# Optimization experiments

Measured on AMD Instinct MI355X. Metric: run time of the kernel, lower is better.

## Reference

```python
import jax, jax.numpy as jnp
import numpy as np

D_MODEL = 1024
HIDDEN = 512
NUM_EXPERTS = 16
TOP_K = 2
CAP_FACTOR = 1.25
ALPHA = 0.01


def setup_inputs() -> dict:
    key = jax.random.key(0)
    ks = jax.random.split(key, 10)
    s_in = 1.0 / np.sqrt(D_MODEL)
    s_h = 1.0 / np.sqrt(HIDDEN)
    return {
        "x": jax.random.normal(ks[0], (4, 4096, D_MODEL), dtype=jnp.float32),
        "gate_w": jax.random.normal(ks[1], (D_MODEL, NUM_EXPERTS), dtype=jnp.float32) * s_in,
        "gate_b": jnp.zeros((NUM_EXPERTS,), dtype=jnp.float32),
        "gp_w": jax.random.normal(ks[2], (NUM_EXPERTS, D_MODEL, HIDDEN), dtype=jnp.float32) * s_in,
        "gp_b": jnp.zeros((NUM_EXPERTS, HIDDEN), dtype=jnp.float32),
        "up_w": jax.random.normal(ks[3], (NUM_EXPERTS, D_MODEL, HIDDEN), dtype=jnp.float32) * s_in,
        "up_b": jnp.zeros((NUM_EXPERTS, HIDDEN), dtype=jnp.float32),
        "dp_w": jax.random.normal(ks[4], (NUM_EXPERTS, HIDDEN, D_MODEL), dtype=jnp.float32) * s_h,
        "dp_b": jnp.zeros((NUM_EXPERTS, D_MODEL), dtype=jnp.float32),
    }


def reference(x, gate_w, gate_b, gp_w, gp_b, up_w, up_b, dp_w, dp_b):
    B, S, D = x.shape
    T = B * S
    xf = x.reshape(T, D)

    # --- MoEGate ---
    logits = xf @ gate_w + gate_b                      # [T, E]
    scores = jax.nn.softmax(logits, axis=-1)
    topk_w, topk_i = jax.lax.top_k(scores, TOP_K)      # [T, K]
    # norm_topk_prob=True in DeepSeekMoE
    topk_w = topk_w / (jnp.sum(topk_w, axis=-1, keepdims=True) + 1e-9)

    one_hot = jax.nn.one_hot(topk_i, NUM_EXPERTS, dtype=jnp.float32)  # [T, K, E]
    load = jnp.sum(one_hot, axis=(0, 1))               # [E]
    capacity = CAP_FACTOR * (T * TOP_K) / NUM_EXPERTS
    capacity_penalty = jnp.sum(jax.nn.relu(load - capacity)) / NUM_EXPERTS / T
    aux_loss = ALPHA * capacity_penalty

    # combine weight of expert e for each token: [T, E]
    comb = jnp.einsum("tke,tk->te", one_hot, topk_w)

    # --- dispatch/combine (dense per-expert, weighted by comb) ---
    out = jnp.zeros_like(xf)
    for e in range(NUM_EXPERTS):
        # Expert: down_proj(gate_proj(x) * silu(up_proj(x)))
        h = (xf @ gp_w[e] + gp_b[e]) * jax.nn.silu(xf @ up_w[e] + up_b[e])
        y = h @ dp_w[e] + dp_b[e]
        out = out + comb[:, e:e + 1] * y

    return out.reshape(B, S, D), aux_loss
```

## Files before the change

kernel.cpp:

```cpp
#include <hip/hip_runtime.h>
#include <hip/hip_bf16.h>
#include <math.h>

#define T_TOK 16384
#define DMODEL 1024
#define HID 512
#define NEXP 16
#define NASSIGN (T_TOK * 2)
#define HIST_BLK 64
#define TOK_PER_BLK (T_TOK / HIST_BLK)
#define NMB_MAX 143

typedef __bf16 bf16_8 __attribute__((ext_vector_type(8)));
typedef __bf16 bf16_4 __attribute__((ext_vector_type(4)));
typedef float f32_4 __attribute__((ext_vector_type(4)));

__device__ __forceinline__ void gload16(const __bf16* g, __bf16* l) {
  __builtin_amdgcn_global_load_lds(
      (const __attribute__((address_space(1))) void*)g,
      (__attribute__((address_space(3))) void*)l, 16, 0, 0);
}

__global__ __launch_bounds__(256) void gate_compute_kernel(
    const float* __restrict__ x, const float* __restrict__ gw, const float* __restrict__ gb,
    __bf16* __restrict__ xb, int* __restrict__ topk_idx, float2* __restrict__ topk_w)
{
  __shared__ __align__(16) float gws[4 * 1024 * 4];

  int tid = threadIdx.x;
#pragma unroll
  for (int i = 0; i < 16; ++i) {
    int c = i * 256 + tid;
    f32_4 v = ((const f32_4*)gw)[c];
    ((f32_4*)gws)[((c & 3) << 10) | (c >> 2)] = v;
  }
  __syncthreads();

  int wave = tid >> 6, lane = tid & 63;
  int tbase = blockIdx.x * 32 + wave * 8;

#pragma unroll 1
  for (int pass = 0; pass < 2; ++pass) {
    int t0 = tbase + pass * 4;
    const float* xr0 = x + (size_t)t0 * DMODEL;
    const float* xr1 = xr0 + DMODEL;
    const float* xr2 = xr1 + DMODEL;
    const float* xr3 = xr2 + DMODEL;
    __bf16* xw0 = xb + (size_t)t0 * DMODEL;
    __bf16* xw1 = xw0 + DMODEL;
    __bf16* xw2 = xw1 + DMODEL;
    __bf16* xw3 = xw2 + DMODEL;

    f32_4 acc0[4], acc1[4], acc2[4], acc3[4];
    {
      f32_4 z = {0.f, 0.f, 0.f, 0.f};
#pragma unroll
      for (int g = 0; g < 4; ++g) { acc0[g] = z; acc1[g] = z; acc2[g] = z; acc3[g] = z; }
    }

#pragma unroll
    for (int j = 0; j < 16; ++j) {
      int k = j * 64 + lane;
      float xv0 = xr0[k], xv1 = xr1[k], xv2 = xr2[k], xv3 = xr3[k];
      xw0[k] = (__bf16)xv0;
      xw1[k] = (__bf16)xv1;
      xw2[k] = (__bf16)xv2;
      xw3[k] = (__bf16)xv3;
      f32_4 w0 = ((const f32_4*)gws)[k];
      f32_4 w1 = ((const f32_4*)gws)[1024 + k];
      f32_4 w2 = ((const f32_4*)gws)[2048 + k];
      f32_4 w3 = ((const f32_4*)gws)[3072 + k];
      acc0[0] += xv0 * w0; acc0[1] += xv0 * w1; acc0[2] += xv0 * w2; acc0[3] += xv0 * w3;
      acc1[0] += xv1 * w0; acc1[1] += xv1 * w1; acc1[2] += xv1 * w2; acc1[3] += xv1 * w3;
      acc2[0] += xv2 * w0; acc2[1] += xv2 * w1; acc2[2] += xv2 * w2; acc2[3] += xv2 * w3;
      acc3[0] += xv3 * w0; acc3[1] += xv3 * w1; acc3[2] += xv3 * w2; acc3[3] += xv3 * w3;
    }

#pragma unroll
    for (int g = 0; g < 4; ++g)
#pragma unroll
      for (int w = 0; w < 4; ++w) {
        float v0 = acc0[g][w], v1 = acc1[g][w], v2 = acc2[g][w], v3 = acc3[g][w];
#pragma unroll
        for (int s = 32; s; s >>= 1) {
          v0 += __shfl_xor(v0, s, 64);
          v1 += __shfl_xor(v1, s, 64);
          v2 += __shfl_xor(v2, s, 64);
          v3 += __shfl_xor(v3, s, 64);
        }
        acc0[g][w] = v0; acc1[g][w] = v1; acc2[g][w] = v2; acc3[g][w] = v3;
      }

    int ti = lane & 3;
    float sc[16];
#pragma unroll
    for (int e = 0; e < 16; ++e) {
      int g = e >> 2, w = e & 3;
      float v = ti == 0 ? acc0[g][w] : ti == 1 ? acc1[g][w] : ti == 2 ? acc2[g][w] : acc3[g][w];
      sc[e] = v + gb[e];
    }
    float mx = -1e30f;
#pragma unroll
    for (int e = 0; e < 16; ++e) mx = fmaxf(mx, sc[e]);
    float Z = 0.f;
#pragma unroll
    for (int e = 0; e < 16; ++e) { sc[e] = expf(sc[e] - mx); Z += sc[e]; }
    int i0 = 0; float s0 = sc[0];
#pragma unroll
    for (int e = 1; e < 16; ++e) if (sc[e] > s0) { s0 = sc[e]; i0 = e; }
    int i1 = -1; float s1 = -1e30f;
#pragma unroll
    for (int e = 0; e < 16; ++e) if (e != i0 && sc[e] > s1) { s1 = sc[e]; i1 = e; }
    s0 /= Z; s1 /= Z;
    float dn = s0 + s1 + 1e-9f;
    if (lane < 4) {
      int t = t0 + ti;
      topk_idx[t] = i0 | (i1 << 8);
      topk_w[t] = make_float2(s0 / dn, s1 / dn);
    }
  }
}

__global__ __launch_bounds__(256) void hist_kernel(
    const int* __restrict__ topk_idx, int* __restrict__ block_hist)
{
  __shared__ int cnt[NEXP];
  int tid = threadIdx.x;
  if (tid < NEXP) cnt[tid] = 0;
  __syncthreads();
  int t = blockIdx.x * TOK_PER_BLK + tid;
  int p = topk_idx[t];
  atomicAdd(&cnt[p & 0xff], 1);
  atomicAdd(&cnt[p >> 8], 1);
  __syncthreads();
  if (tid < NEXP) block_hist[blockIdx.x * NEXP + tid] = cnt[tid];
}

__global__ void scan2_kernel(const int* __restrict__ block_hist,
                             int* __restrict__ counts, int* __restrict__ offsets,
                             int* __restrict__ block_base, int* __restrict__ mb_tab,
                             int* __restrict__ nmb, float* __restrict__ aux_out)
{
  __shared__ int cl[NEXP];
  int lane = threadIdx.x;
  if (lane < NEXP) {
    int s = 0;
    for (int b = 0; b < HIST_BLK; ++b) s += block_hist[b * NEXP + lane];
    cl[lane] = s;
    counts[lane] = s;
  }
  __syncthreads();
  if (lane < NEXP) {
    int off = 0;
    for (int e = 0; e < lane; ++e) off += cl[e];
    offsets[lane] = off;
    int base = off;
    for (int b = 0; b < HIST_BLK; ++b) {
      block_base[b * NEXP + lane] = base;
      base += block_hist[b * NEXP + lane];
    }
  }
  if (lane == 0) {
    int tot = 0; float pen = 0.f;
    const float cap = 1.25f * (float)(T_TOK * 2) / (float)NEXP;
    for (int e = 0; e < NEXP; ++e) {
      tot += cl[e];
      float ld = (float)cl[e] - cap;
      pen += ld > 0.f ? ld : 0.f;
    }
    offsets[NEXP] = tot;
    aux_out[0] = 0.01f * pen / (float)NEXP / (float)T_TOK;
    int idx = 0;
    for (int e = 0; e < NEXP; ++e) {
      int nb = (cl[e] + 255) >> 8;
      for (int b = 0; b < nb; ++b) mb_tab[idx++] = (e << 8) | b;
    }
    nmb[0] = idx;
  }
}

__global__ __launch_bounds__(256) void scatter_kernel(
    const int* __restrict__ topk_idx, const int* __restrict__ block_base,
    int* __restrict__ tok_list, int2* __restrict__ tok_slots)
{
  __shared__ int base[NEXP];
  int tid = threadIdx.x;
  if (tid < NEXP) base[tid] = block_base[blockIdx.x * NEXP + tid];
  __syncthreads();
  int t = blockIdx.x * TOK_PER_BLK + tid;
  int p = topk_idx[t];
  int i0 = p & 0xff, i1 = p >> 8;
  int p0 = atomicAdd(&base[i0], 1);
  tok_list[p0] = t;
  int p1 = atomicAdd(&base[i1], 1);
  tok_list[p1] = t;
  tok_slots[t] = make_int2(p0, p1);
}

__global__ __launch_bounds__(256) void transpose_w1_kernel(const float* __restrict__ gp,
                                                           const float* __restrict__ up,
                                                           __bf16* __restrict__ wb1)
{
  __shared__ float tile[32][33];
  int ez = blockIdx.z;
  int e = ez >> 1, isup = ez & 1;
  const float* in = isup ? up : gp;
  int c0 = blockIdx.x * 32, r0 = blockIdx.y * 32;
  const float* src = in + ((size_t)e * 1024 + r0) * 512 + c0;
#pragma unroll
  for (int i = 0; i < 4; ++i) {
    int r = threadIdx.y + i * 8;
    tile[r][threadIdx.x] = src[(size_t)r * 512 + threadIdx.x];
  }
  __syncthreads();
#pragma unroll
  for (int i = 0; i < 4; ++i) {
    int cc = threadIdx.y + i * 8;
    int np = 2 * c0 + 2 * (cc & ~15) + (cc & 15) + 16 * isup;
    wb1[((size_t)e * 1024 + np) * 1024 + r0 + threadIdx.x] = (__bf16)tile[threadIdx.x][cc];
  }
}

__global__ __launch_bounds__(256) void transpose_dp_kernel(const float* __restrict__ in,
                                                           __bf16* __restrict__ out)
{
  __shared__ float tile[32][33];
  int e = blockIdx.z;
  int c0 = blockIdx.x * 32, r0 = blockIdx.y * 32;
  const float* src = in + ((size_t)e * 512 + r0) * 1024 + c0;
#pragma unroll
  for (int i = 0; i < 4; ++i) {
    int r = threadIdx.y + i * 8;
    tile[r][threadIdx.x] = src[(size_t)r * 1024 + threadIdx.x];
  }
  __syncthreads();
  __bf16* dst = out + ((size_t)e * 1024 + c0) * 512 + r0;
#pragma unroll
  for (int i = 0; i < 4; ++i) {
    int c = threadIdx.y + i * 8;
    dst[(size_t)c * 512 + threadIdx.x] = (__bf16)tile[threadIdx.x][c];
  }
}


#define PHASE_MID()                                          \
  __builtin_amdgcn_sched_barrier(0);                         \
  __builtin_amdgcn_s_barrier();                              \
  asm volatile("s_waitcnt lgkmcnt(0)" ::: "memory");         \
  __builtin_amdgcn_sched_barrier(0);                         \
  __builtin_amdgcn_s_setprio(1);

#define PHASE_END()                                          \
  __builtin_amdgcn_s_setprio(0);                             \
  __builtin_amdgcn_sched_barrier(0);                         \
  __builtin_amdgcn_s_barrier();

#define MF(mi, ni, a, b) acc[mi][ni] = __builtin_amdgcn_mfma_f32_16x16x32_bf16(a, b, acc[mi][ni], 0, 0, 0)

#define STAGE_A(b, kt) {                                          \
    gload16(ga0 + (kt) * 32, lds + (b) * 16384 + tid * 8);        \
    gload16(ga1 + (kt) * 32, lds + (b) * 16384 + 4096 + tid * 8); }
#define STAGE_B(b, kt) {                                          \
    gload16(gb0 + (kt) * 32, lds + (b) * 16384 + 8192 + tid * 8); \
    gload16(gb1 + (kt) * 32, lds + (b) * 16384 + 12288 + tid * 8); }

#define GTILE(ktv, STG)                                                           \
  {                                                                               \
    const __bf16* A_ = lds + ((ktv) & 1) * 16384;                                 \
    const __bf16* B_ = A_ + 8192;                                                 \
    bf16_8 af0, af1, af2, af3, bf0, bf1, bf2, bf3;                                \
    af0 = *(const bf16_8*)(A_ + abase + 0 * 512 + sq);                            \
    af1 = *(const bf16_8*)(A_ + abase + 1 * 512 + sq);                            \
    af2 = *(const bf16_8*)(A_ + abase + 2 * 512 + sq);                            \
    af3 = *(const bf16_8*)(A_ + abase + 3 * 512 + sq);                            \
    bf0 = *(const bf16_8*)(B_ + bbase + 0 * 512 + sq);                            \
    bf1 = *(const bf16_8*)(B_ + bbase + 1 * 512 + sq);                            \
    bf2 = *(const bf16_8*)(B_ + bbase + 2 * 512 + sq);                            \
    bf3 = *(const bf16_8*)(B_ + bbase + 3 * 512 + sq);                            \
    if (STG) STAGE_A(((ktv) + 1) & 1, (ktv) + 1);                                 \
    PHASE_MID();                                                                  \
    MF(0, 0, af0, bf0); MF(0, 1, af0, bf1); MF(0, 2, af0, bf2); MF(0, 3, af0, bf3); \
    MF(1, 0, af1, bf0); MF(1, 1, af1, bf1); MF(1, 2, af1, bf2); MF(1, 3, af1, bf3); \
    MF(2, 0, af2, bf0); MF(2, 1, af2, bf1); MF(2, 2, af2, bf2); MF(2, 3, af2, bf3); \
    MF(3, 0, af3, bf0); MF(3, 1, af3, bf1); MF(3, 2, af3, bf2); MF(3, 3, af3, bf3); \
    PHASE_END();                                                                  \
    af0 = *(const bf16_8*)(A_ + abase + 4 * 512 + sq);                            \
    af1 = *(const bf16_8*)(A_ + abase + 5 * 512 + sq);                            \
    af2 = *(const bf16_8*)(A_ + abase + 6 * 512 + sq);                            \
    af3 = *(const bf16_8*)(A_ + abase + 7 * 512 + sq);                            \
    if (STG) STAGE_B(((ktv) + 1) & 1, (ktv) + 1);                                 \
    PHASE_MID();                                                                  \
    MF(4, 0, af0, bf0); MF(4, 1, af0, bf1); MF(4, 2, af0, bf2); MF(4, 3, af0, bf3); \
    MF(5, 0, af1, bf0); MF(5, 1, af1, bf1); MF(5, 2, af1, bf2); MF(5, 3, af1, bf3); \
    MF(6, 0, af2, bf0); MF(6, 1, af2, bf1); MF(6, 2, af2, bf2); MF(6, 3, af2, bf3); \
    MF(7, 0, af3, bf0); MF(7, 1, af3, bf1); MF(7, 2, af3, bf2); MF(7, 3, af3, bf3); \
    __builtin_amdgcn_s_setprio(0);                                                \
    __builtin_amdgcn_sched_barrier(0);                                            \
    if (STG) { asm volatile("s_waitcnt vmcnt(0)" ::: "memory"); }                 \
    __builtin_amdgcn_sched_barrier(0);                                            \
    __builtin_amdgcn_s_barrier();                                                 \
  }

template<int KTILES>
__device__ __forceinline__ void gemm8w(
    const __bf16* ga0, const __bf16* ga1,
    const __bf16* gb0, const __bf16* gb1,
    __bf16* lds, f32_4 (&acc)[8][4])
{
  const int tid = threadIdx.x;
  const int wid = tid >> 6, wr = wid >> 2, wc = wid & 3;
  const int lane = tid & 63, quad = lane >> 4, l16 = lane & 15;
  const int sq = (quad ^ ((l16 >> 1) & 3)) * 8;
  const int abase = (wr * 128 + l16) * 32;
  const int bbase = (wc * 64 + l16) * 32;

  STAGE_A(0, 0); STAGE_B(0, 0);
  asm volatile("s_waitcnt vmcnt(0)" ::: "memory");
  __builtin_amdgcn_sched_barrier(0);
  __builtin_amdgcn_s_barrier();

#pragma unroll 1
  for (int kt = 0; kt < KTILES - 1; ++kt) {
    GTILE(kt, 1);
  }
  GTILE(KTILES - 1, 0);
}

__global__ __launch_bounds__(512, 2) void ffn1_kernel(
    const __bf16* __restrict__ xb, const __bf16* __restrict__ wb1,
    const float* __restrict__ gp_b, const float* __restrict__ up_b,
    const int* __restrict__ counts, const int* __restrict__ offsets,
    const int* __restrict__ tok_list, const int* __restrict__ mb_tab,
    const int* __restrict__ nmb, __bf16* __restrict__ h)
{
  __shared__ __align__(16) __bf16 lds[2 * 16384];
  __shared__ int toks[256];

  int lin = blockIdx.y * 4 + blockIdx.x;
  int xcd = lin & 7, sub = lin >> 3;
  int wg = (xcd < 4 ? xcd * 72 : 288 + (xcd - 4) * 71) + sub;
  int y = wg >> 2, xn = wg & 3;
  if (y >= nmb[0]) return;
  int me = mb_tab[y];
  int e = me >> 8;
  int m0 = (me & 255) << 8;
  int cnt = counts[e], offe = offsets[e];
  int n0 = xn * 256;

  int tid = threadIdx.x;
  if (tid < 256) {
    int r = m0 + tid;
    toks[tid] = tok_list[offe + (r < cnt ? r : cnt - 1)];
  }
  __syncthreads();

  int rr = tid >> 2;
  int ko = ((tid & 3) ^ ((rr >> 1) & 3)) * 8;

  const __bf16* ga0 = xb + (size_t)toks[rr] * DMODEL + ko;
  const __bf16* ga1 = xb + (size_t)toks[128 + rr] * DMODEL + ko;
  const __bf16* gb0 = wb1 + ((size_t)e * 1024 + n0 + rr) * DMODEL + ko;
  const __bf16* gb1 = wb1 + ((size_t)e * 1024 + n0 + 128 + rr) * DMODEL + ko;

  f32_4 acc[8][4];
  {
    f32_4 z = {0.f, 0.f, 0.f, 0.f};
#pragma unroll
    for (int a = 0; a < 8; ++a)
#pragma unroll
      for (int b = 0; b < 4; ++b) acc[a][b] = z;
  }

  gemm8w<DMODEL / 32>(ga0, ga1, gb0, gb1, lds, acc);

  int wid = tid >> 6, wr = wid >> 2, wc = wid & 3;
  int lane = tid & 63, quad = lane >> 4, l16 = lane & 15;

#pragma unroll
  for (int mi = 0; mi < 8; ++mi)
#pragma unroll
    for (int j = 0; j < 2; ++j) {
      int c = (n0 >> 1) + wc * 32 + j * 16 + l16;
      float gbias = gp_b[e * HID + c];
      float ubias = up_b[e * HID + c];
#pragma unroll
      for (int rg = 0; rg < 4; ++rg) {
        int r = m0 + wr * 128 + mi * 16 + quad * 4 + rg;
        if (r < cnt) {
          float g = acc[mi][2 * j][rg] + gbias;
          float u = acc[mi][2 * j + 1][rg] + ubias;
          float sw = u / (1.f + expf(-u));
          h[(size_t)(offe + r) * HID + c] = (__bf16)(g * sw);
        }
      }
    }
}

__global__ __launch_bounds__(512, 2) void ffn2_kernel(
    const __bf16* __restrict__ h, const __bf16* __restrict__ dpb, const float* __restrict__ dp_b,
    const int* __restrict__ counts, const int* __restrict__ offsets,
    const int* __restrict__ mb_tab, const int* __restrict__ nmb,
    __bf16* __restrict__ ybuf)
{
  __shared__ __align__(16) __bf16 lds[2 * 16384];

  int lin = blockIdx.y * 4 + blockIdx.x;
  int xcd = lin & 7, sub = lin >> 3;
  int wg = (xcd < 4 ? xcd * 72 : 288 + (xcd - 4) * 71) + sub;
  int y = wg >> 2, xn = wg & 3;
  if (y >= nmb[0]) return;
  int me = mb_tab[y];
  int e = me >> 8;
  int m0 = (me & 255) << 8;
  int cnt = counts[e], offe = offsets[e];
  int n0 = xn * 256;

  int tid = threadIdx.x;
  int rr = tid >> 2;
  int ko = ((tid & 3) ^ ((rr >> 1) & 3)) * 8;

  int ra0 = m0 + rr;        if (ra0 >= cnt) ra0 = cnt - 1;
  int ra1 = m0 + 128 + rr;  if (ra1 >= cnt) ra1 = cnt - 1;
  const __bf16* ga0 = h + (size_t)(offe + ra0) * HID + ko;
  const __bf16* ga1 = h + (size_t)(offe + ra1) * HID + ko;
  const __bf16* gb0 = dpb + ((size_t)e * DMODEL + n0 + rr) * HID + ko;
  const __bf16* gb1 = dpb + ((size_t)e * DMODEL + n0 + 128 + rr) * HID + ko;

  f32_4 acc[8][4];
  {
    f32_4 z = {0.f, 0.f, 0.f, 0.f};
#pragma unroll
    for (int a = 0; a < 8; ++a)
#pragma unroll
      for (int b = 0; b < 4; ++b) acc[a][b] = z;
  }

  gemm8w<HID / 32>(ga0, ga1, gb0, gb1, lds, acc);

  int wid = tid >> 6, wr = wid >> 2, wc = wid & 3;
  int lane = tid & 63, quad = lane >> 4, l16 = lane & 15;

#pragma unroll
  for (int mi = 0; mi < 8; ++mi)
#pragma unroll
    for (int ni = 0; ni < 4; ++ni) {
      int n = n0 + wc * 64 + ni * 16 + l16;
      float bias = dp_b[e * DMODEL + n];
#pragma unroll
      for (int rg = 0; rg < 4; ++rg) {
        int r = m0 + wr * 128 + mi * 16 + quad * 4 + rg;
        if (r < cnt) {
          float v = acc[mi][ni][rg] + bias;
          ybuf[(size_t)(offe + r) * DMODEL + n] = (__bf16)v;
        }
      }
    }
}

__global__ __launch_bounds__(256) void combine_kernel(
    const __bf16* __restrict__ ybuf, const int2* __restrict__ tok_slots,
    const float2* __restrict__ topk_w, float* __restrict__ out)
{
  int tid = threadIdx.x;
  int t = blockIdx.x * 2 + (tid >> 7);
  int d = (tid & 127) * 8;
  int2 sl = tok_slots[t];
  float2 w = topk_w[t];
  bf16_8 y0 = *(const bf16_8*)(ybuf + (size_t)sl.x * DMODEL + d);
  bf16_8 y1 = *(const bf16_8*)(ybuf + (size_t)sl.y * DMODEL + d);
  float* o = out + (size_t)t * DMODEL + d;
  f32_4 r0, r1;
#pragma unroll
  for (int i = 0; i < 4; ++i) r0[i] = w.x * (float)y0[i] + w.y * (float)y1[i];
#pragma unroll
  for (int i = 0; i < 4; ++i) r1[i] = w.x * (float)y0[4 + i] + w.y * (float)y1[4 + i];
  *(f32_4*)o = r0;
  *(f32_4*)(o + 4) = r1;
}

extern "C" void kernel_launch(void* const* d_in, const int* in_sizes, int n_in,
                              void* d_out, int out_size, void* d_ws, size_t ws_size,
                              hipStream_t stream)
{
  const float* x      = (const float*)d_in[0];
  const float* gate_w = (const float*)d_in[1];
  const float* gate_b = (const float*)d_in[2];
  const float* gp_w   = (const float*)d_in[3];
  const float* gp_b   = (const float*)d_in[4];
  const float* up_w   = (const float*)d_in[5];
  const float* up_b   = (const float*)d_in[6];
  const float* dp_w   = (const float*)d_in[7];
  const float* dp_b   = (const float*)d_in[8];

  char* ws = (char*)d_ws;
  size_t o = 0;
  __bf16* xb  = (__bf16*)(ws + o); o += (size_t)T_TOK * DMODEL * 2;
  __bf16* wb1 = (__bf16*)(ws + o); o += (size_t)NEXP * 1024 * DMODEL * 2;
  __bf16* dpb = (__bf16*)(ws + o); o += (size_t)NEXP * DMODEL * HID * 2;
  __bf16* hbuf = (__bf16*)(ws + o); o += (size_t)NASSIGN * HID * 2;
  int*   tok_list = (int*)(ws + o); o += (size_t)NASSIGN * 4;
  int2*  tok_slots = (int2*)(ws + o); o += (size_t)T_TOK * 8;
  int*   topk_idx = (int*)(ws + o); o += (size_t)T_TOK * 4;
  float2* topk_w  = (float2*)(ws + o); o += (size_t)T_TOK * 8;
  int*   block_hist = (int*)(ws + o); o += (size_t)HIST_BLK * NEXP * 4;
  int*   block_base = (int*)(ws + o); o += (size_t)HIST_BLK * NEXP * 4;
  int*   counts   = (int*)(ws + o); o += 64;
  int*   offsets  = (int*)(ws + o); o += 128;
  int*   mb_tab   = (int*)(ws + o); o += 4 * 160;
  int*   nmb      = (int*)(ws + o); o += 64;
  __bf16* ybuf = (__bf16*)ws;

  float* out = (float*)d_out;
  float* aux = out + (size_t)T_TOK * DMODEL;

  gate_compute_kernel<<<T_TOK / 32, 256, 0, stream>>>(x, gate_w, gate_b, xb, topk_idx, topk_w);
  hist_kernel<<<HIST_BLK, TOK_PER_BLK, 0, stream>>>(topk_idx, block_hist);
  scan2_kernel<<<1, 64, 0, stream>>>(block_hist, counts, offsets, block_base, mb_tab, nmb, aux);
  scatter_kernel<<<HIST_BLK, TOK_PER_BLK, 0, stream>>>(topk_idx, block_base, tok_list, tok_slots);
  transpose_w1_kernel<<<dim3(512 / 32, 1024 / 32, 2 * NEXP), dim3(32, 8), 0, stream>>>(gp_w, up_w, wb1);
  transpose_dp_kernel<<<dim3(1024 / 32, 512 / 32, NEXP), dim3(32, 8), 0, stream>>>(dp_w, dpb);
  ffn1_kernel<<<dim3(4, NMB_MAX, 1), 512, 0, stream>>>(xb, wb1, gp_b, up_b,
                                                       counts, offsets, tok_list, mb_tab, nmb, hbuf);
  ffn2_kernel<<<dim3(4, NMB_MAX, 1), 512, 0, stream>>>(hbuf, dpb, dp_b,
                                                       counts, offsets, mb_tab, nmb, ybuf);
  combine_kernel<<<T_TOK / 2, 256, 0, stream>>>(ybuf, tok_slots, topk_w, out);
}
```

Measured before the change: 487.5 us.

## Double K tile to 64 and simplify GEMM pipeline to one barrier per tile

The grouped expert GEMM mainloop now stages K=64 slices instead of K=32, with a new 8-wide XOR swizzle and four row pointers per operand. The old split-phase schedule with interleaved barriers, explicit lgkmcnt waits and sched_barriers is replaced by one prefetch at the top of the tile and a single __syncthreads at the end. The goal is to halve barrier and loop overhead per unit of MFMA work. In exchange LDS use per block doubles to 128KB, which may block two workgroups per CU, and the compiler now controls memory waits instead of the hand-tuned scheduling.

After: 457.8 us. 1.06x faster.

```diff
diff --git a/kernel.cpp b/kernel.cpp
--- a/kernel.cpp
+++ b/kernel.cpp
@@ -243,81 +243,66 @@
 }
 
 
-#define PHASE_MID()                                          \
-  __builtin_amdgcn_sched_barrier(0);                         \
-  __builtin_amdgcn_s_barrier();                              \
-  asm volatile("s_waitcnt lgkmcnt(0)" ::: "memory");         \
-  __builtin_amdgcn_sched_barrier(0);                         \
-  __builtin_amdgcn_s_setprio(1);
-
-#define PHASE_END()                                          \
-  __builtin_amdgcn_s_setprio(0);                             \
-  __builtin_amdgcn_sched_barrier(0);                         \
-  __builtin_amdgcn_s_barrier();
-
 #define MF(mi, ni, a, b) acc[mi][ni] = __builtin_amdgcn_mfma_f32_16x16x32_bf16(a, b, acc[mi][ni], 0, 0, 0)
 
-#define STAGE_A(b, kt) {                                          \
-    gload16(ga0 + (kt) * 32, lds + (b) * 16384 + tid * 8);        \
-    gload16(ga1 + (kt) * 32, lds + (b) * 16384 + 4096 + tid * 8); }
-#define STAGE_B(b, kt) {                                          \
-    gload16(gb0 + (kt) * 32, lds + (b) * 16384 + 8192 + tid * 8); \
-    gload16(gb1 + (kt) * 32, lds + (b) * 16384 + 12288 + tid * 8); }
+#define STAGE_T(b, kt) {                                             \
+    gload16(ga0 + (kt) * 64, lds + (b) * 32768 + tid * 8);           \
+    gload16(ga1 + (kt) * 64, lds + (b) * 32768 + 4096 + tid * 8);    \
+    gload16(ga2 + (kt) * 64, lds + (b) * 32768 + 8192 + tid * 8);    \
+    gload16(ga3 + (kt) * 64, lds + (b) * 32768 + 12288 + tid * 8);   \
+    gload16(gb0 + (kt) * 64, lds + (b) * 32768 + 16384 + tid * 8);   \
+    gload16(gb1 + (kt) * 64, lds + (b) * 32768 + 20480 + tid * 8);   \
+    gload16(gb2 + (kt) * 64, lds + (b) * 32768 + 24576 + tid * 8);   \
+    gload16(gb3 + (kt) * 64, lds + (b) * 32768 + 28672 + tid * 8); }
 
 #define GTILE(ktv, STG)                                                           \
   {                                                                               \
-    const __bf16* A_ = lds + ((ktv) & 1) * 16384;                                 \
-    const __bf16* B_ = A_ + 8192;                                                 \
-    bf16_8 af0, af1, af2, af3, bf0, bf1, bf2, bf3;                                \
-    af0 = *(const bf16_8*)(A_ + abase + 0 * 512 + sq);                            \
-    af1 = *(const bf16_8*)(A_ + abase + 1 * 512 + sq);                            \
-    af2 = *(const bf16_8*)(A_ + abase + 2 * 512 + sq);                            \
-    af3 = *(const bf16_8*)(A_ + abase + 3 * 512 + sq);                            \
-    bf0 = *(const bf16_8*)(B_ + bbase + 0 * 512 + sq);                            \
-    bf1 = *(const bf16_8*)(B_ + bbase + 1 * 512 + sq);                            \
-    bf2 = *(const bf16_8*)(B_ + bbase + 2 * 512 + sq);                            \
-    bf3 = *(const bf16_8*)(B_ + bbase + 3 * 512 + sq);                            \
-    if (STG) STAGE_A(((ktv) + 1) & 1, (ktv) + 1);                                 \
-    PHASE_MID();                                                                  \
-    MF(0, 0, af0, bf0); MF(0, 1, af0, bf1); MF(0, 2, af0, bf2); MF(0, 3, af0, bf3); \
-    MF(1, 0, af1, bf0); MF(1, 1, af1, bf1); MF(1, 2, af1, bf2); MF(1, 3, af1, bf3); \
-    MF(2, 0, af2, bf0); MF(2, 1, af2, bf1); MF(2, 2, af2, bf2); MF(2, 3, af2, bf3); \
-    MF(3, 0, af3, bf0); MF(3, 1, af3, bf1); MF(3, 2, af3, bf2); MF(3, 3, af3, bf3); \
-    PHASE_END();                                                                  \
-    af0 = *(const bf16_8*)(A_ + abase + 4 * 512 + sq);                            \
-    af1 = *(const bf16_8*)(A_ + abase + 5 * 512 + sq);                            \
-    af2 = *(const bf16_8*)(A_ + abase + 6 * 512 + sq);                            \
-    af3 = *(const bf16_8*)(A_ + abase + 7 * 512 + sq);                            \
-    if (STG) STAGE_B(((ktv) + 1) & 1, (ktv) + 1);                                 \
-    PHASE_MID();                                                                  \
-    MF(4, 0, af0, bf0); MF(4, 1, af0, bf1); MF(4, 2, af0, bf2); MF(4, 3, af0, bf3); \
-    MF(5, 0, af1, bf0); MF(5, 1, af1, bf1); MF(5, 2, af1, bf2); MF(5, 3, af1, bf3); \
-    MF(6, 0, af2, bf0); MF(6, 1, af2, bf1); MF(6, 2, af2, bf2); MF(6, 3, af2, bf3); \
-    MF(7, 0, af3, bf0); MF(7, 1, af3, bf1); MF(7, 2, af3, bf2); MF(7, 3, af3, bf3); \
+    const __bf16* A_ = lds + ((ktv) & 1) * 32768;                                 \
+    const __bf16* B_ = A_ + 16384;                                                \
+    if (STG) STAGE_T(((ktv) + 1) & 1, (ktv) + 1);                                 \
+    bf16_8 af[8], bf[4];                                                          \
+    _Pragma("unroll")                                                             \
+    for (int mi = 0; mi < 8; ++mi)                                                \
+      af[mi] = *(const bf16_8*)(A_ + abase + mi * 1024 + c0);                     \
+    _Pragma("unroll")                                                             \
+    for (int ni = 0; ni < 4; ++ni)                                                \
+      bf[ni] = *(const bf16_8*)(B_ + bbase + ni * 1024 + c0);                     \
+    __builtin_amdgcn_s_setprio(1);                                                \
+    _Pragma("unroll")                                                             \
+    for (int mi = 0; mi < 8; ++mi) {                                              \
+      MF(mi, 0, af[mi], bf[0]); MF(mi, 1, af[mi], bf[1]);                         \
+      MF(mi, 2, af[mi], bf[2]); MF(mi, 3, af[mi], bf[3]);                         \
+    }                                                                             \
+    _Pragma("unroll")                                                             \
+    for (int mi = 0; mi < 8; ++mi)                                                \
+      af[mi] = *(const bf16_8*)(A_ + abase + mi * 1024 + (c0 ^ 32));              \
+    _Pragma("unroll")                                                             \
+    for (int ni = 0; ni < 4; ++ni)                                                \
+      bf[ni] = *(const bf16_8*)(B_ + bbase + ni * 1024 + (c0 ^ 32));              \
+    _Pragma("unroll")                                                             \
+    for (int mi = 0; mi < 8; ++mi) {                                              \
+      MF(mi, 0, af[mi], bf[0]); MF(mi, 1, af[mi], bf[1]);                         \
+      MF(mi, 2, af[mi], bf[2]); MF(mi, 3, af[mi], bf[3]);                         \
+    }                                                                             \
     __builtin_amdgcn_s_setprio(0);                                                \
-    __builtin_amdgcn_sched_barrier(0);                                            \
-    if (STG) { asm volatile("s_waitcnt vmcnt(0)" ::: "memory"); }                 \
-    __builtin_amdgcn_sched_barrier(0);                                            \
-    __builtin_amdgcn_s_barrier();                                                 \
+    __syncthreads();                                                              \
   }
 
 template<int KTILES>
 __device__ __forceinline__ void gemm8w(
-    const __bf16* ga0, const __bf16* ga1,
-    const __bf16* gb0, const __bf16* gb1,
+    const __bf16* ga0, const __bf16* ga1, const __bf16* ga2, const __bf16* ga3,
+    const __bf16* gb0, const __bf16* gb1, const __bf16* gb2, const __bf16* gb3,
     __bf16* lds, f32_4 (&acc)[8][4])
 {
   const int tid = threadIdx.x;
   const int wid = tid >> 6, wr = wid >> 2, wc = wid & 3;
   const int lane = tid & 63, quad = lane >> 4, l16 = lane & 15;
-  const int sq = (quad ^ ((l16 >> 1) & 3)) * 8;
-  const int abase = (wr * 128 + l16) * 32;
-  const int bbase = (wc * 64 + l16) * 32;
-
-  STAGE_A(0, 0); STAGE_B(0, 0);
-  asm volatile("s_waitcnt vmcnt(0)" ::: "memory");
-  __builtin_amdgcn_sched_barrier(0);
-  __builtin_amdgcn_s_barrier();
+  const int c0 = (quad ^ (l16 & 7)) * 8;
+  const int abase = (wr * 128 + l16) * 64;
+  const int bbase = (wc * 64 + l16) * 64;
+
+  STAGE_T(0, 0);
+  __syncthreads();
 
 #pragma unroll 1
   for (int kt = 0; kt < KTILES - 1; ++kt) {
@@ -333,7 +318,7 @@
     const int* __restrict__ tok_list, const int* __restrict__ mb_tab,
     const int* __restrict__ nmb, __bf16* __restrict__ h)
 {
-  __shared__ __align__(16) __bf16 lds[2 * 16384];
+  __shared__ __align__(16) __bf16 lds[2 * 32768];
   __shared__ int toks[256];
 
   int lin = blockIdx.y * 4 + blockIdx.x;
@@ -354,13 +339,17 @@
   }
   __syncthreads();
 
-  int rr = tid >> 2;
-  int ko = ((tid & 3) ^ ((rr >> 1) & 3)) * 8;
+  int rr = tid >> 3;
+  int ko = ((tid & 7) ^ (rr & 7)) * 8;
 
   const __bf16* ga0 = xb + (size_t)toks[rr] * DMODEL + ko;
-  const __bf16* ga1 = xb + (size_t)toks[128 + rr] * DMODEL + ko;
+  const __bf16* ga1 = xb + (size_t)toks[64 + rr] * DMODEL + ko;
+  const __bf16* ga2 = xb + (size_t)toks[128 + rr] * DMODEL + ko;
+  const __bf16* ga3 = xb + (size_t)toks[192 + rr] * DMODEL + ko;
   const __bf16* gb0 = wb1 + ((size_t)e * 1024 + n0 + rr) * DMODEL + ko;
-  const __bf16* gb1 = wb1 + ((size_t)e * 1024 + n0 + 128 + rr) * DMODEL + ko;
+  const __bf16* gb1 = wb1 + ((size_t)e * 1024 + n0 + 64 + rr) * DMODEL + ko;
+  const __bf16* gb2 = wb1 + ((size_t)e * 1024 + n0 + 128 + rr) * DMODEL + ko;
+  const __bf16* gb3 = wb1 + ((size_t)e * 1024 + n0 + 192 + rr) * DMODEL + ko;
 
   f32_4 acc[8][4];
   {
@@ -371,7 +360,7 @@
       for (int b = 0; b < 4; ++b) acc[a][b] = z;
   }
 
-  gemm8w<DMODEL / 32>(ga0, ga1, gb0, gb1, lds, acc);
+  gemm8w<DMODEL / 64>(ga0, ga1, ga2, ga3, gb0, gb1, gb2, gb3, lds, acc);
 
   int wid = tid >> 6, wr = wid >> 2, wc = wid & 3;
   int lane = tid & 63, quad = lane >> 4, l16 = lane & 15;
@@ -402,7 +391,7 @@
     const int* __restrict__ mb_tab, const int* __restrict__ nmb,
     __bf16* __restrict__ ybuf)
 {
-  __shared__ __align__(16) __bf16 lds[2 * 16384];
+  __shared__ __align__(16) __bf16 lds[2 * 32768];
 
   int lin = blockIdx.y * 4 + blockIdx.x;
   int xcd = lin & 7, sub = lin >> 3;
@@ -416,15 +405,21 @@
   int n0 = xn * 256;
 
   int tid = threadIdx.x;
-  int rr = tid >> 2;
-  int ko = ((tid & 3) ^ ((rr >> 1) & 3)) * 8;
+  int rr = tid >> 3;
+  int ko = ((tid & 7) ^ (rr & 7)) * 8;
 
   int ra0 = m0 + rr;        if (ra0 >= cnt) ra0 = cnt - 1;
-  int ra1 = m0 + 128 + rr;  if (ra1 >= cnt) ra1 = cnt - 1;
+  int ra1 = m0 + 64 + rr;   if (ra1 >= cnt) ra1 = cnt - 1;
+  int ra2 = m0 + 128 + rr;  if (ra2 >= cnt) ra2 = cnt - 1;
+  int ra3 = m0 + 192 + rr;  if (ra3 >= cnt) ra3 = cnt - 1;
   const __bf16* ga0 = h + (size_t)(offe + ra0) * HID + ko;
   const __bf16* ga1 = h + (size_t)(offe + ra1) * HID + ko;
+  const __bf16* ga2 = h + (size_t)(offe + ra2) * HID + ko;
+  const __bf16* ga3 = h + (size_t)(offe + ra3) * HID + ko;
   const __bf16* gb0 = dpb + ((size_t)e * DMODEL + n0 + rr) * HID + ko;
-  const __bf16* gb1 = dpb + ((size_t)e * DMODEL + n0 + 128 + rr) * HID + ko;
+  const __bf16* gb1 = dpb + ((size_t)e * DMODEL + n0 + 64 + rr) * HID + ko;
+  const __bf16* gb2 = dpb + ((size_t)e * DMODEL + n0 + 128 + rr) * HID + ko;
+  const __bf16* gb3 = dpb + ((size_t)e * DMODEL + n0 + 192 + rr) * HID + ko;
 
   f32_4 acc[8][4];
   {
@@ -435,7 +430,7 @@
       for (int b = 0; b < 4; ++b) acc[a][b] = z;
   }
 
-  gemm8w<HID / 32>(ga0, ga1, gb0, gb1, lds, acc);
+  gemm8w<HID / 64>(ga0, ga1, ga2, ga3, gb0, gb1, gb2, gb3, lds, acc);
 
   int wid = tid >> 6, wr = wid >> 2, wc = wid & 3;
   int lane = tid & 63, quad = lane >> 4, l16 = lane & 15;
```
